# Performance work log

Hardware: AMD Instinct MI355X
Metric: run time of the kernel (lower is better)

The kernel has to match this reference:

```python
import jax, jax.numpy as jnp
import numpy as np

H = 100  # hidden size


def _lstm_final_hidden(x, W_ih, W_hh, b_ih, b_hh):
    # x: [B, T, 4] -> final hidden state h_T: [B, H]
    B, T, _ = x.shape
    # Precompute input contribution for all time steps: [B, T, 4H]
    xW = jnp.einsum('btf,gf->btg', x, W_ih) + b_ih + b_hh
    xW = jnp.transpose(xW, (1, 0, 2))  # [T, B, 4H] for scan over time

    def step(carry, xt):
        h, c = carry
        gates = xt + h @ W_hh.T  # [B, 4H]
        i, f, g, o = jnp.split(gates, 4, axis=-1)  # torch gate order: i, f, g, o
        c = jax.nn.sigmoid(f) * c + jax.nn.sigmoid(i) * jnp.tanh(g)
        h = jax.nn.sigmoid(o) * jnp.tanh(c)
        return (h, c), None

    h0 = jnp.zeros((B, H), dtype=x.dtype)
    (hT, _), _ = jax.lax.scan(step, (h0, h0), xW)
    return hT


def setup_inputs() -> dict:
    key = jax.random.key(0)
    k1, k2, k3, k4, k5 = jax.random.split(key, 5)
    n_cells, T = 4096, 128
    short_ttf = jax.random.normal(k1, (n_cells, 3, T, 4), dtype=jnp.float32)
    W_ih = jax.random.normal(k2, (4 * H, 4), dtype=jnp.float32) * 0.1
    # torch init: uniform(-0.05, 0.05) for weight_hh
    W_hh = jax.random.uniform(k3, (4 * H, H), dtype=jnp.float32, minval=-0.05, maxval=0.05)
    b_ih = jax.random.normal(k4, (4 * H,), dtype=jnp.float32) * 0.1
    b_hh = jax.random.normal(k5, (4 * H,), dtype=jnp.float32) * 0.1
    return {"short_ttf": short_ttf, "W_ih": W_ih, "W_hh": W_hh, "b_ih": b_ih, "b_hh": b_hh}


def reference(short_ttf, W_ih, W_hh, b_ih, b_hh):
    # short_ttf: [n_cells, 3, T, 4]. Each of the 3 sub-sequences per cell is run
    # through the same LSTM; last-step hidden states are concatenated -> [n_cells, 3H].
    n_cells, three, T, F = short_ttf.shape
    x = short_ttf.reshape(n_cells * three, T, F)  # batch all sequences together
    hT = _lstm_final_hidden(x, W_ih, W_hh, b_ih, b_hh)  # [n_cells*3, H]
    return hT.reshape(n_cells, three * H)  # [n_cells, 300]
```

## Files before the change

### kernel.cpp

```cpp
#include <hip/hip_runtime.h>
#include <cstdint>


#define H_UNITS 100
#define T_STEPS 128
#define S_BLK   16
#define NSEQ    12288
#define NBLK    (NSEQ / S_BLK)
#define NTILE   25
#define KSTR    136

typedef __attribute__((ext_vector_type(8))) _Float16 halfx8;
typedef __attribute__((ext_vector_type(8))) unsigned short ushortx8;
typedef __attribute__((ext_vector_type(4))) float floatx4;

__device__ __forceinline__ unsigned short f32_to_f16u(float x) {
    _Float16 h = (_Float16)x;
    return __builtin_bit_cast(unsigned short, h);
}
__device__ __forceinline__ float f16u_to_f32(unsigned short u) {
    _Float16 h = __builtin_bit_cast(_Float16, u);
    return (float)h;
}
__device__ __forceinline__ float fsigm(float x) {
    return __builtin_amdgcn_rcpf(1.0f + __expf(-x));
}
__device__ __forceinline__ float ftanh(float x) {
    return 1.0f - 2.0f * __builtin_amdgcn_rcpf(1.0f + __expf(2.0f * x));
}

__global__ void lstm_prep_pack(const float* __restrict__ W_ih,
                               const float* __restrict__ W_hh,
                               const float* __restrict__ b_ih,
                               const float* __restrict__ b_hh,
                               ushortx8* __restrict__ Bpack) {
    int t = blockIdx.x * 256 + threadIdx.x;
    if (t >= NTILE * 4 * 64) return;
    int lane = t & 63;
    int kc   = (t >> 6) & 3;
    int tile = t >> 8;
    int m    = lane & 15;
    int n  = (m & 3) * 100 + tile * 4 + (m >> 2);
    int k0 = kc * 32 + ((lane >> 4) & 3) * 8;
    ushortx8 v;
#pragma unroll
    for (int j = 0; j < 8; ++j) {
        int k = k0 + j;
        unsigned short w = 0;
        if (k < 100) {
            w = f32_to_f16u(W_hh[n * 100 + k]);
        } else if (k < 104) {
            w = f32_to_f16u(W_ih[n * 4 + (k - 100)]);
        } else if (k < 108) {
            float wf = W_ih[n * 4 + (k - 104)];
            unsigned short hi = f32_to_f16u(wf);
            w = f32_to_f16u(wf - f16u_to_f32(hi));
        } else if (k == 108) {
            float b = b_ih[n] + b_hh[n];
            w = f32_to_f16u(b);
        } else if (k == 109) {
            float b = b_ih[n] + b_hh[n];
            unsigned short hi = f32_to_f16u(b);
            w = f32_to_f16u(b - f16u_to_f32(hi));
        }
        v[j] = w;
    }
    Bpack[t] = v;
}

__global__ void __launch_bounds__(256, 3)
lstm_main(const float* __restrict__ x, const ushortx8* __restrict__ Bpack,
          float* __restrict__ out) {
    __shared__ __align__(16) unsigned short s_A[2][2 * 16 * KSTR];
    __shared__ __align__(16) ushortx8       s_Wk0[NTILE * 64];

    const int tid  = threadIdx.x;
    const int lane = tid & 63;
    const int wave = tid >> 6;
    const int seq0 = blockIdx.x * S_BLK;
    const int m    = lane & 15;
    const int quad = lane >> 4;

    halfx8 wfrag[7][3];
#pragma unroll
    for (int it = 0; it < 7; ++it) {
        int tile = wave + it * 4;
        if (tile < NTILE) {
#pragma unroll
            for (int kc = 0; kc < 3; ++kc)
                wfrag[it][kc] = __builtin_bit_cast(halfx8, Bpack[(tile * 4 + kc + 1) * 64 + lane]);
        }
    }
    for (int i = tid; i < NTILE * 64; i += 256)
        s_Wk0[i] = Bpack[(i >> 6) * 256 + (i & 63)];

    const int rs = tid & 15, rc = tid >> 4;
    const float* xb = x + (size_t)(seq0 + rs) * (T_STEPS * 4) + (rc & 3);

    for (int i = tid; i < (2 * 2 * 16 * KSTR) / 2; i += 256)
        ((unsigned int*)s_A)[i] = 0u;
    float x0 = 0.0f;
    if (tid < 128) x0 = xb[0];
    __syncthreads();
    if (tid < 128) {
        unsigned short hi = f32_to_f16u(x0);
        if (rc < 4) {
            s_A[0][rs * KSTR + 100 + rc]        = hi;
            s_A[0][(16 + rs) * KSTR + 100 + rc] = f32_to_f16u(x0 - f16u_to_f32(hi));
        } else {
            s_A[0][(16 + rs) * KSTR + 100 + rc] = hi;
        }
    } else if (tid < 160) {
        int d = tid - 128;
        s_A[d >> 4][(d & 15) * KSTR + 108] = 0x3C00;
    } else if (tid < 192) {
        int d = tid - 160;
        s_A[d >> 4][(16 + (d & 15)) * KSTR + 109] = 0x3C00;
    }

    float c_reg[7];
#pragma unroll
    for (int it = 0; it < 7; ++it) c_reg[it] = 0.0f;

    const int aOffHi = m * KSTR + quad * 8;
    const int aOffLo = (16 + m) * KSTR + 96 + quad * 8;

    for (int t = 0; t < T_STEPS; ++t) {
        const int bR = t & 1;
        float xnext = 0.0f;
        if (tid < 128) {
            int tn = t + 1; if (tn > T_STEPS - 1) tn = T_STEPS - 1;
            xnext = xb[tn * 4];
        }
        __syncthreads();

        const unsigned short* base  = s_A[bR];
        unsigned short*       baseW = s_A[bR ^ 1];
        halfx8 hh[4], hl3;
#pragma unroll
        for (int kc = 0; kc < 4; ++kc)
            hh[kc] = *(const halfx8*)(base + aOffHi + kc * 32);
        hl3 = *(const halfx8*)(base + aOffLo);

        const bool last = (t == T_STEPS - 1);
#pragma unroll
        for (int it = 0; it < 7; ++it) {
            int tile = wave + it * 4;
            if (tile < NTILE) {
                halfx8 w0 = __builtin_bit_cast(halfx8, s_Wk0[tile * 64 + lane]);
                floatx4 acc = {0.0f, 0.0f, 0.0f, 0.0f};
                acc = __builtin_amdgcn_mfma_f32_16x16x32_f16(w0,           hh[0], acc, 0, 0, 0);
                acc = __builtin_amdgcn_mfma_f32_16x16x32_f16(wfrag[it][0], hh[1], acc, 0, 0, 0);
                acc = __builtin_amdgcn_mfma_f32_16x16x32_f16(wfrag[it][1], hh[2], acc, 0, 0, 0);
                acc = __builtin_amdgcn_mfma_f32_16x16x32_f16(wfrag[it][2], hh[3], acc, 0, 0, 0);
                acc = __builtin_amdgcn_mfma_f32_16x16x32_f16(wfrag[it][2], hl3,  acc, 0, 0, 0);
                float c = fsigm(acc[1]) * c_reg[it] + fsigm(acc[0]) * ftanh(acc[2]);
                c_reg[it] = c;
                float h = fsigm(acc[3]) * ftanh(c);
                int j = tile * 4 + quad;
                if (!last) {
                    baseW[m * KSTR + j] = f32_to_f16u(h);
                } else {
                    out[(size_t)(seq0 + m) * H_UNITS + j] = h;
                }
            }
        }
        if (tid < 128 && !last) {
            unsigned short hi = f32_to_f16u(xnext);
            if (rc < 4) {
                baseW[rs * KSTR + 100 + rc]        = hi;
                baseW[(16 + rs) * KSTR + 100 + rc] = f32_to_f16u(xnext - f16u_to_f32(hi));
            } else {
                baseW[(16 + rs) * KSTR + 100 + rc] = hi;
            }
        }
    }
}

extern "C" void kernel_launch(void* const* d_in, const int* in_sizes, int n_in,
                              void* d_out, int out_size, void* d_ws, size_t ws_size,
                              hipStream_t stream) {
    const float* x    = (const float*)d_in[0];
    const float* W_ih = (const float*)d_in[1];
    const float* W_hh = (const float*)d_in[2];
    const float* b_ih = (const float*)d_in[3];
    const float* b_hh = (const float*)d_in[4];
    ushortx8* Bpack = (ushortx8*)d_ws;

    lstm_prep_pack<<<25, 256, 0, stream>>>(W_ih, W_hh, b_ih, b_hh, Bpack);
    lstm_main<<<NBLK, 256, 0, stream>>>(x, Bpack, (float*)d_out);
}
```

Baseline: 335.9 us.

## Fold split-precision terms into one K block and fuse gate activations

Repacks the K dimension so the input-weight hi/lo and bias compensation terms all fit inside the 128-wide K range. This drops the separate low-part A row block and the fifth MFMA per tile. Gate nonlinearities are rewritten as combined exp/reciprocal expressions, so each cell uses fewer rcp operations, with a clamp added to keep the tanh exp from overflowing. The 25th tile is handled explicitly on wave 0. An extra block barrier per time step is added, which adds some synchronization cost.

```diff
diff --git a/kernel.cpp b/kernel.cpp
--- a/kernel.cpp
+++ b/kernel.cpp
@@ -21,12 +21,6 @@
 __device__ __forceinline__ float f16u_to_f32(unsigned short u) {
     _Float16 h = __builtin_bit_cast(_Float16, u);
     return (float)h;
-}
-__device__ __forceinline__ float fsigm(float x) {
-    return __builtin_amdgcn_rcpf(1.0f + __expf(-x));
-}
-__device__ __forceinline__ float ftanh(float x) {
-    return 1.0f - 2.0f * __builtin_amdgcn_rcpf(1.0f + __expf(2.0f * x));
 }
 
 __global__ void lstm_prep_pack(const float* __restrict__ W_ih,
@@ -49,16 +43,16 @@
         unsigned short w = 0;
         if (k < 100) {
             w = f32_to_f16u(W_hh[n * 100 + k]);
-        } else if (k < 104) {
-            w = f32_to_f16u(W_ih[n * 4 + (k - 100)]);
         } else if (k < 108) {
-            float wf = W_ih[n * 4 + (k - 104)];
+            w = f32_to_f16u(W_ih[n * 4 + ((k - 100) & 3)]);
+        } else if (k < 112) {
+            float wf = W_ih[n * 4 + (k - 108)];
             unsigned short hi = f32_to_f16u(wf);
             w = f32_to_f16u(wf - f16u_to_f32(hi));
-        } else if (k == 108) {
+        } else if (k == 112) {
             float b = b_ih[n] + b_hh[n];
             w = f32_to_f16u(b);
-        } else if (k == 109) {
+        } else if (k == 113) {
             float b = b_ih[n] + b_hh[n];
             unsigned short hi = f32_to_f16u(b);
             w = f32_to_f16u(b - f16u_to_f32(hi));
@@ -71,7 +65,7 @@
 __global__ void __launch_bounds__(256, 3)
 lstm_main(const float* __restrict__ x, const ushortx8* __restrict__ Bpack,
           float* __restrict__ out) {
-    __shared__ __align__(16) unsigned short s_A[2][2 * 16 * KSTR];
+    __shared__ __align__(16) unsigned short s_A[2][16 * KSTR];
     __shared__ __align__(16) ushortx8       s_Wk0[NTILE * 64];
 
     const int tid  = threadIdx.x;
@@ -97,33 +91,35 @@
     const int rs = tid & 15, rc = tid >> 4;
     const float* xb = x + (size_t)(seq0 + rs) * (T_STEPS * 4) + (rc & 3);
 
-    for (int i = tid; i < (2 * 2 * 16 * KSTR) / 2; i += 256)
+    for (int i = tid; i < (2 * 16 * KSTR) / 2; i += 256)
         ((unsigned int*)s_A)[i] = 0u;
     float x0 = 0.0f;
     if (tid < 128) x0 = xb[0];
     __syncthreads();
     if (tid < 128) {
-        unsigned short hi = f32_to_f16u(x0);
         if (rc < 4) {
-            s_A[0][rs * KSTR + 100 + rc]        = hi;
-            s_A[0][(16 + rs) * KSTR + 100 + rc] = f32_to_f16u(x0 - f16u_to_f32(hi));
+            unsigned short hi = f32_to_f16u(x0);
+            s_A[0][rs * KSTR + 100 + rc] = hi;
+            s_A[0][rs * KSTR + 108 + rc] = hi;
         } else {
-            s_A[0][(16 + rs) * KSTR + 100 + rc] = hi;
+            float xv = x0;
+            unsigned short hi = f32_to_f16u(xv);
+            s_A[0][rs * KSTR + 104 + (rc - 4)] = f32_to_f16u(xv - f16u_to_f32(hi));
         }
     } else if (tid < 160) {
         int d = tid - 128;
-        s_A[d >> 4][(d & 15) * KSTR + 108] = 0x3C00;
+        s_A[d >> 4][(d & 15) * KSTR + 112] = 0x3C00;
     } else if (tid < 192) {
         int d = tid - 160;
-        s_A[d >> 4][(16 + (d & 15)) * KSTR + 109] = 0x3C00;
-    }
-
-    float c_reg[7];
-#pragma unroll
-    for (int it = 0; it < 7; ++it) c_reg[it] = 0.0f;
-
-    const int aOffHi = m * KSTR + quad * 8;
-    const int aOffLo = (16 + m) * KSTR + 96 + quad * 8;
+        s_A[d >> 4][(d & 15) * KSTR + 113] = 0x3C00;
+    }
+
+    float c_reg[6];
+#pragma unroll
+    for (int it = 0; it < 6; ++it) c_reg[it] = 0.0f;
+    float c24 = 0.0f;
+
+    const int aOff = m * KSTR + quad * 8;
 
     for (int t = 0; t < T_STEPS; ++t) {
         const int bR = t & 1;
@@ -136,44 +132,60 @@
 
         const unsigned short* base  = s_A[bR];
         unsigned short*       baseW = s_A[bR ^ 1];
-        halfx8 hh[4], hl3;
+        halfx8 hh[4];
 #pragma unroll
         for (int kc = 0; kc < 4; ++kc)
-            hh[kc] = *(const halfx8*)(base + aOffHi + kc * 32);
-        hl3 = *(const halfx8*)(base + aOffLo);
+            hh[kc] = *(const halfx8*)(base + aOff + kc * 32);
 
         const bool last = (t == T_STEPS - 1);
-#pragma unroll
-        for (int it = 0; it < 7; ++it) {
-            int tile = wave + it * 4;
-            if (tile < NTILE) {
-                halfx8 w0 = __builtin_bit_cast(halfx8, s_Wk0[tile * 64 + lane]);
-                floatx4 acc = {0.0f, 0.0f, 0.0f, 0.0f};
-                acc = __builtin_amdgcn_mfma_f32_16x16x32_f16(w0,           hh[0], acc, 0, 0, 0);
-                acc = __builtin_amdgcn_mfma_f32_16x16x32_f16(wfrag[it][0], hh[1], acc, 0, 0, 0);
-                acc = __builtin_amdgcn_mfma_f32_16x16x32_f16(wfrag[it][1], hh[2], acc, 0, 0, 0);
-                acc = __builtin_amdgcn_mfma_f32_16x16x32_f16(wfrag[it][2], hh[3], acc, 0, 0, 0);
-                acc = __builtin_amdgcn_mfma_f32_16x16x32_f16(wfrag[it][2], hl3,  acc, 0, 0, 0);
-                float c = fsigm(acc[1]) * c_reg[it] + fsigm(acc[0]) * ftanh(acc[2]);
-                c_reg[it] = c;
-                float h = fsigm(acc[3]) * ftanh(c);
-                int j = tile * 4 + quad;
-                if (!last) {
-                    baseW[m * KSTR + j] = f32_to_f16u(h);
-                } else {
-                    out[(size_t)(seq0 + m) * H_UNITS + j] = h;
-                }
+
+        auto docell = [&](int tile, halfx8 w1, halfx8 w2, halfx8 w3, float& cm) {
+            halfx8 w0 = __builtin_bit_cast(halfx8, s_Wk0[tile * 64 + lane]);
+            floatx4 acc = {0.0f, 0.0f, 0.0f, 0.0f};
+            acc = __builtin_amdgcn_mfma_f32_16x16x32_f16(w0, hh[0], acc, 0, 0, 0);
+            acc = __builtin_amdgcn_mfma_f32_16x16x32_f16(w1, hh[1], acc, 0, 0, 0);
+            acc = __builtin_amdgcn_mfma_f32_16x16x32_f16(w2, hh[2], acc, 0, 0, 0);
+            acc = __builtin_amdgcn_mfma_f32_16x16x32_f16(w3, hh[3], acc, 0, 0, 0);
+            float ei = __expf(acc[0]);
+            float ef = __expf(acc[1]);
+            float eg = __expf(2.0f * acc[2]);
+            float eo = __expf(acc[3]);
+            float a  = 1.0f + ei, b = 1.0f + ef;
+            float d  = eg + 1.0f, e2 = eg - 1.0f;
+            float q  = a * d;
+            float r  = __builtin_amdgcn_rcpf(q * b);
+            float nm = fmaf(ef * q, cm, (ei * b) * e2);
+            float c  = nm * r;
+            cm = c;
+            float cc = fminf(c, 40.0f);
+            float ec = __expf(2.0f * cc);
+            float r2 = __builtin_amdgcn_rcpf((1.0f + eo) * (ec + 1.0f));
+            float h  = (eo * (ec - 1.0f)) * r2;
+            int j = tile * 4 + quad;
+            if (!last) {
+                baseW[m * KSTR + j] = f32_to_f16u(h);
+            } else {
+                out[(size_t)(seq0 + m) * H_UNITS + j] = h;
             }
-        }
+        };
+
+#pragma unroll
+        for (int it = 0; it < 6; ++it)
+            docell(wave + it * 4, wfrag[it][0], wfrag[it][1], wfrag[it][2], c_reg[it]);
+        if (wave == 0)
+            docell(24, wfrag[6][0], wfrag[6][1], wfrag[6][2], c24);
+
         if (tid < 128 && !last) {
-            unsigned short hi = f32_to_f16u(xnext);
             if (rc < 4) {
-                baseW[rs * KSTR + 100 + rc]        = hi;
-                baseW[(16 + rs) * KSTR + 100 + rc] = f32_to_f16u(xnext - f16u_to_f32(hi));
+                unsigned short hi = f32_to_f16u(xnext);
+                baseW[rs * KSTR + 100 + rc] = hi;
+                baseW[rs * KSTR + 108 + rc] = hi;
             } else {
-                baseW[(16 + rs) * KSTR + 100 + rc] = hi;
+                unsigned short hi = f32_to_f16u(xnext);
+                baseW[rs * KSTR + 104 + (rc - 4)] = f32_to_f16u(xnext - f16u_to_f32(hi));
             }
         }
+        __syncthreads();
     }
 }
 
```

After: 324.4 us. 3.4% less time.
